# Kernel optimization log

Measured on AMD Instinct MI355X. Metric: run time of the kernel, lower is better.

## Reference

```python
import jax, jax.numpy as jnp
import numpy as np

EPS = 1e-8


def setup_inputs() -> dict:
    key = jax.random.key(0)
    k1, k2, k3, k4, k5 = jax.random.split(key, 5)
    N, B, T, D = 8, 2, 2048, 2048
    F = 4 * D
    blocks = jax.random.normal(k1, (N, B, T, D), dtype=jnp.float32)
    partial_block = jax.random.normal(k2, (B, T, D), dtype=jnp.float32)
    proj_w = jax.random.normal(k3, (D,), dtype=jnp.float32) * 0.02
    norm_scale = jnp.ones((D,), dtype=jnp.float32)
    ffn_w1 = jax.random.normal(k4, (D, F), dtype=jnp.float32) * 0.02
    ffn_w2 = jax.random.normal(k5, (F, D), dtype=jnp.float32) * 0.02
    return {
        "blocks": blocks,
        "partial_block": partial_block,
        "proj_w": proj_w,
        "norm_scale": norm_scale,
        "ffn_w1": ffn_w1,
        "ffn_w2": ffn_w2,
    }


def reference(blocks, partial_block, proj_w, norm_scale, ffn_w1, ffn_w2):
    # Stack completed blocks with current partial sum: V [N1, B, T, D]
    V = jnp.concatenate([blocks, partial_block[None]], axis=0)
    # RMSNorm over D (keys)
    rms = jnp.sqrt(jnp.mean(V * V, axis=-1, keepdims=True) + EPS)
    K = norm_scale * V / rms
    # Pseudo-query dot-product logits [N1, B, T], softmax over blocks (axis 0)
    logits = jnp.einsum('nbtd,d->nbt', K, proj_w)
    alpha = jax.nn.softmax(logits, axis=0)
    # Weighted sum of raw values -> new hidden state h [B, T, D]
    h = jnp.einsum('nbt,nbtd->btd', alpha, V)
    # Sublayer: standard FFN (D -> 4D gelu -> D)
    f_out = jax.nn.gelu(h @ ffn_w1) @ ffn_w2
    # layer_number % block_size != 0 branch: accumulate partial sum
    new_partial = partial_block + f_out
    return h, new_partial
```

## Files before the change

kernel.cpp:

```cpp
#include <hip/hip_runtime.h>

typedef unsigned short ushort_t;
typedef __bf16 bf16x8 __attribute__((ext_vector_type(8)));
typedef float f32x4 __attribute__((ext_vector_type(4)));

#define NB 8
#define BB 2
#define TT 2048
#define DD 2048
#define FF 8192
#define MM (BB * TT)
#define BTD ((size_t)BB * TT * DD)

__device__ __forceinline__ unsigned short f2bf(float f) {
  unsigned int u = __float_as_uint(f);
  u += 0x7FFFu + ((u >> 16) & 1u);
  return (unsigned short)(u >> 16);
}

__device__ __forceinline__ float gelu_tanh(float x) {
  float u = 0.7978845608028654f * (x + 0.044715f * x * x * x);
  float e = __expf(2.0f * u);
  float th = 1.0f - 2.0f / (e + 1.0f);
  return 0.5f * x * (1.0f + th);
}

#define ASYNC_COPY16(gp, lp)                                                   \
  __builtin_amdgcn_global_load_lds(                                            \
      (__attribute__((address_space(1))) void*)(gp),                           \
      (__attribute__((address_space(3))) void*)(lp), 16, 0, 0)

__global__ __launch_bounds__(256) void transpose_conv(
    const float* __restrict__ in, ushort_t* __restrict__ out, int R, int C) {
  __shared__ float tile[32][33];
  const int tx = threadIdx.x & 31, ty = threadIdx.x >> 5;
  const int r0 = blockIdx.y * 32, c0 = blockIdx.x * 32;
#pragma unroll
  for (int i = 0; i < 32; i += 8)
    tile[ty + i][tx] = in[(size_t)(r0 + ty + i) * C + (c0 + tx)];
  __syncthreads();
#pragma unroll
  for (int i = 0; i < 32; i += 8)
    out[(size_t)(c0 + ty + i) * R + (r0 + tx)] = f2bf(tile[tx][ty + i]);
}

__global__ __launch_bounds__(256) void attn_fuse(
    const float* __restrict__ blocks, const float* __restrict__ partial,
    const float* __restrict__ proj_w, const float* __restrict__ norm_scale,
    float* __restrict__ h_out, ushort_t* __restrict__ h_bf) {
  const int t = threadIdx.x;
  const int bt = blockIdx.x;
  const size_t rowoff = (size_t)bt * DD;
  const int d0 = t * 4;

  float w[8];
  {
    float4 ns = *(const float4*)(norm_scale + d0);
    float4 pw = *(const float4*)(proj_w + d0);
    w[0] = ns.x * pw.x; w[1] = ns.y * pw.y; w[2] = ns.z * pw.z; w[3] = ns.w * pw.w;
    ns = *(const float4*)(norm_scale + 1024 + d0);
    pw = *(const float4*)(proj_w + 1024 + d0);
    w[4] = ns.x * pw.x; w[5] = ns.y * pw.y; w[6] = ns.z * pw.z; w[7] = ns.w * pw.w;
  }

  float ss[9], dt[9];
#pragma unroll
  for (int n = 0; n < 9; ++n) {
    const float* rp = (n < 8) ? (blocks + (size_t)n * BTD + rowoff)
                              : (partial + rowoff);
    float4 v0 = *(const float4*)(rp + d0);
    float4 v1 = *(const float4*)(rp + 1024 + d0);
    ss[n] = v0.x * v0.x + v0.y * v0.y + v0.z * v0.z + v0.w * v0.w +
            v1.x * v1.x + v1.y * v1.y + v1.z * v1.z + v1.w * v1.w;
    dt[n] = v0.x * w[0] + v0.y * w[1] + v0.z * w[2] + v0.w * w[3] +
            v1.x * w[4] + v1.y * w[5] + v1.z * w[6] + v1.w * w[7];
  }

  __shared__ float red[2][9][4];
  const int lane = t & 63, wv = t >> 6;
#pragma unroll
  for (int n = 0; n < 9; ++n) {
    float a = ss[n], c = dt[n];
#pragma unroll
    for (int off = 32; off > 0; off >>= 1) {
      a += __shfl_down(a, off, 64);
      c += __shfl_down(c, off, 64);
    }
    if (lane == 0) { red[0][n][wv] = a; red[1][n][wv] = c; }
  }
  __syncthreads();
  __shared__ float logit_s[9];
  if (t < 9) {
    float a = red[0][t][0] + red[0][t][1] + red[0][t][2] + red[0][t][3];
    float c = red[1][t][0] + red[1][t][1] + red[1][t][2] + red[1][t][3];
    logit_s[t] = c * rsqrtf(a * (1.0f / (float)DD) + 1e-8f);
  }
  __syncthreads();

  float lg[9], mx = -1e30f;
#pragma unroll
  for (int n = 0; n < 9; ++n) { lg[n] = logit_s[n]; mx = fmaxf(mx, lg[n]); }
  float den = 0.0f;
#pragma unroll
  for (int n = 0; n < 9; ++n) { lg[n] = __expf(lg[n] - mx); den += lg[n]; }
  const float inv = 1.0f / den;

  float h[8] = {0, 0, 0, 0, 0, 0, 0, 0};
#pragma unroll
  for (int n = 0; n < 9; ++n) {
    const float* rp = (n < 8) ? (blocks + (size_t)n * BTD + rowoff)
                              : (partial + rowoff);
    float4 v0 = *(const float4*)(rp + d0);
    float4 v1 = *(const float4*)(rp + 1024 + d0);
    const float a = lg[n] * inv;
    h[0] += a * v0.x; h[1] += a * v0.y; h[2] += a * v0.z; h[3] += a * v0.w;
    h[4] += a * v1.x; h[5] += a * v1.y; h[6] += a * v1.z; h[7] += a * v1.w;
  }

  float4 o0 = {h[0], h[1], h[2], h[3]}, o1 = {h[4], h[5], h[6], h[7]};
  *(float4*)(h_out + rowoff + d0) = o0;
  *(float4*)(h_out + rowoff + 1024 + d0) = o1;
  uint2 p0, p1;
  p0.x = (unsigned)f2bf(h[0]) | ((unsigned)f2bf(h[1]) << 16);
  p0.y = (unsigned)f2bf(h[2]) | ((unsigned)f2bf(h[3]) << 16);
  p1.x = (unsigned)f2bf(h[4]) | ((unsigned)f2bf(h[5]) << 16);
  p1.y = (unsigned)f2bf(h[6]) | ((unsigned)f2bf(h[7]) << 16);
  *(uint2*)(h_bf + rowoff + d0) = p0;
  *(uint2*)(h_bf + rowoff + 1024 + d0) = p1;
}

template <int BN, int EPI>
__global__ __launch_bounds__(512) void gemm256(
    const ushort_t* __restrict__ A, const ushort_t* __restrict__ BT,
    const int K, const int N, const int GX, ushort_t* __restrict__ Cb,
    const float* __restrict__ addend, float* __restrict__ Cf) {
  constexpr int BM = 256;
  constexpr int WCN = BN / 4;
  constexpr int MF = 8;
  constexpr int NF = WCN / 16;
  constexpr int MH = 4;
  constexpr int CH_B = BN / 128;
  constexpr int ABYTES = BM * 64 * 2;

  __shared__ __align__(16) ushort_t lds0[(BM + BN) * 64];
  __shared__ __align__(16) ushort_t lds1[(BM + BN) * 64];

  const int t = threadIdx.x;
  const int lane = t & 63, wv = t >> 6;
  const int wr = wv >> 2, wc = wv & 3;
  const int fr = lane & 15;

  const int nwg = gridDim.x;
  const int wg = blockIdx.x;
  const int swz = (wg & 7) * (nwg >> 3) + (wg >> 3);
  const int bx = swz % GX, by = swz / GX;
  const int row0 = by * BM, col0 = bx * BN;

  const int sr = t >> 3;
  const int scolb = ((t & 7) * 16) ^ ((sr & 7) << 4);
  const ushort_t* gA = A + (size_t)(row0 + sr) * K + (scolb >> 1);
  const ushort_t* gB = BT + (size_t)(col0 + sr) * K + (scolb >> 1);

#define STAGE(DST, KT)                                                         \
  {                                                                            \
    const int _k0 = (KT)*64;                                                   \
    for (int j = 0; j < 4; ++j)                                                \
      ASYNC_COPY16(gA + (size_t)(j * 64) * K + _k0,                            \
                   &DST[j * 4096 + wv * 512]);                                 \
    for (int j = 0; j < 2 * CH_B; ++j)                                         \
      ASYNC_COPY16(gB + (size_t)(j * 64) * K + _k0,                            \
                   &DST[BM * 64 + j * 4096 + wv * 512]);                       \
  }

  const int s_lane = (fr & 7) << 4;
  const int offk0 = ((lane >> 4) * 16) ^ s_lane;
  const int offk1 = (64 + (lane >> 4) * 16) ^ s_lane;
  const int aoffA = (wr * 128 + fr) * 128;
  int boffB[NF];
#pragma unroll
  for (int n = 0; n < NF; ++n)
    boffB[n] = ABYTES + (wc * WCN + n * 16 + fr) * 128;

  f32x4 acc[MF][NF];
#pragma unroll
  for (int m = 0; m < MF; ++m)
#pragma unroll
    for (int n = 0; n < NF; ++n) {
      f32x4 z = {0.f, 0.f, 0.f, 0.f};
      acc[m][n] = z;
    }

#define TILE(SRC, DST, STAGEKT, DOSTAGE)                                       \
  {                                                                            \
    const char* _L = (const char*)SRC;                                         \
    bf16x8 bfr[NF], afr[MH];                                                   \
                                                     \
    for (int n = 0; n < NF; ++n)                                               \
      bfr[n] = *(const bf16x8*)(_L + boffB[n] + offk0);                        \
    for (int m = 0; m < MH; ++m)                                               \
      afr[m] = *(const bf16x8*)(_L + aoffA + m * 2048 + offk0);                \
    if (DOSTAGE) STAGE(DST, STAGEKT);                                          \
    __builtin_amdgcn_s_barrier();                                              \
    __builtin_amdgcn_s_setprio(1);                                             \
    for (int m = 0; m < MH; ++m)                                               \
      for (int n = 0; n < NF; ++n)                                             \
        acc[m][n] = __builtin_amdgcn_mfma_f32_16x16x32_bf16(afr[m], bfr[n],    \
                                                            acc[m][n], 0, 0, 0); \
    __builtin_amdgcn_s_setprio(0);                                             \
    __builtin_amdgcn_s_barrier();                                              \
                                                     \
    for (int m = 0; m < MH; ++m)                                               \
      afr[m] = *(const bf16x8*)(_L + aoffA + (MH + m) * 2048 + offk0);         \
    __builtin_amdgcn_s_barrier();                                              \
    __builtin_amdgcn_s_setprio(1);                                             \
    for (int m = 0; m < MH; ++m)                                               \
      for (int n = 0; n < NF; ++n)                                             \
        acc[MH + m][n] = __builtin_amdgcn_mfma_f32_16x16x32_bf16(              \
            afr[m], bfr[n], acc[MH + m][n], 0, 0, 0);                          \
    __builtin_amdgcn_s_setprio(0);                                             \
    __builtin_amdgcn_s_barrier();                                              \
                                                     \
    for (int n = 0; n < NF; ++n)                                               \
      bfr[n] = *(const bf16x8*)(_L + boffB[n] + offk1);                        \
    for (int m = 0; m < MH; ++m)                                               \
      afr[m] = *(const bf16x8*)(_L + aoffA + m * 2048 + offk1);                \
    __builtin_amdgcn_s_barrier();                                              \
    __builtin_amdgcn_s_setprio(1);                                             \
    for (int m = 0; m < MH; ++m)                                               \
      for (int n = 0; n < NF; ++n)                                             \
        acc[m][n] = __builtin_amdgcn_mfma_f32_16x16x32_bf16(afr[m], bfr[n],    \
                                                            acc[m][n], 0, 0, 0); \
    __builtin_amdgcn_s_setprio(0);                                             \
    __builtin_amdgcn_s_barrier();                                              \
                                                     \
    for (int m = 0; m < MH; ++m)                                               \
      afr[m] = *(const bf16x8*)(_L + aoffA + (MH + m) * 2048 + offk1);         \
    __builtin_amdgcn_s_barrier();                                              \
    __builtin_amdgcn_s_setprio(1);                                             \
    for (int m = 0; m < MH; ++m)                                               \
      for (int n = 0; n < NF; ++n)                                             \
        acc[MH + m][n] = __builtin_amdgcn_mfma_f32_16x16x32_bf16(              \
            afr[m], bfr[n], acc[MH + m][n], 0, 0, 0);                          \
    __builtin_amdgcn_s_setprio(0);                                             \
    __syncthreads();        \
  }

  STAGE(lds0, 0);
  __syncthreads();

  const int NT = K >> 6;
  for (int kt = 0; kt < NT; kt += 2) {
    TILE(lds0, lds1, kt + 1, (kt + 1 < NT));
    TILE(lds1, lds0, kt + 2, (kt + 2 < NT));
  }

  const int r4 = (lane >> 4) * 4;
#pragma unroll
  for (int m = 0; m < MF; ++m) {
    const int grow = row0 + wr * 128 + m * 16 + r4;
#pragma unroll
    for (int n = 0; n < NF; ++n) {
      const int gcol = col0 + wc * WCN + n * 16 + fr;
#pragma unroll
      for (int r = 0; r < 4; ++r) {
        const float v = acc[m][n][r];
        const size_t idx = (size_t)(grow + r) * N + gcol;
        if (EPI == 0) {
          Cb[idx] = f2bf(gelu_tanh(v));
        } else {
          Cf[idx] = v + addend[idx];
        }
      }
    }
  }
#undef TILE
#undef STAGE
}

extern "C" void kernel_launch(void* const* d_in, const int* in_sizes, int n_in,
                              void* d_out, int out_size, void* d_ws,
                              size_t ws_size, hipStream_t stream) {
  const float* blocks = (const float*)d_in[0];
  const float* partial = (const float*)d_in[1];
  const float* proj_w = (const float*)d_in[2];
  const float* norm_scale = (const float*)d_in[3];
  const float* w1 = (const float*)d_in[4];
  const float* w2 = (const float*)d_in[5];

  float* out = (float*)d_out;
  float* h_out = out;
  float* new_partial = out + BTD;

  char* ws = (char*)d_ws;
  ushort_t* h_bf = (ushort_t*)ws;
  ushort_t* w1T = (ushort_t*)(ws + (size_t)16777216);
  ushort_t* w2T = (ushort_t*)(ws + (size_t)16777216 + 33554432);
  ushort_t* act = (ushort_t*)(ws + (size_t)16777216 + 2 * 33554432ull);

  transpose_conv<<<dim3(FF / 32, DD / 32), 256, 0, stream>>>(w1, w1T, DD, FF);
  transpose_conv<<<dim3(DD / 32, FF / 32), 256, 0, stream>>>(w2, w2T, FF, DD);

  attn_fuse<<<MM, 256, 0, stream>>>(blocks, partial, proj_w, norm_scale, h_out,
                                    h_bf);

  gemm256<256, 0><<<(FF / 256) * (MM / 256), 512, 0, stream>>>(
      h_bf, w1T, DD, FF, FF / 256, act, nullptr, nullptr);
  gemm256<128, 1><<<(DD / 128) * (MM / 256), 512, 0, stream>>>(
      act, w2T, FF, DD, DD / 128, nullptr, partial, new_partial);
}
```

Measured before the change: 423.4 us.

## Split async tile loads into quadrant-ordered chunks with partial vmcnt waits

Measured after the change: 426.9 us. No clear change (+0.8%).

```diff
diff --git a/kernel.cpp b/kernel.cpp
--- a/kernel.cpp
+++ b/kernel.cpp
@@ -23,6 +23,14 @@
   float e = __expf(2.0f * u);
   float th = 1.0f - 2.0f / (e + 1.0f);
   return 0.5f * x * (1.0f + th);
+}
+
+template <int N>
+__device__ __forceinline__ void wait_vmcnt() {
+  if constexpr (N == 0) asm volatile("s_waitcnt vmcnt(0)" ::: "memory");
+  else if constexpr (N == 2) asm volatile("s_waitcnt vmcnt(2)" ::: "memory");
+  else if constexpr (N == 4) asm volatile("s_waitcnt vmcnt(4)" ::: "memory");
+  else if constexpr (N == 6) asm volatile("s_waitcnt vmcnt(6)" ::: "memory");
 }
 
 #define ASYNC_COPY16(gp, lp)                                                   \
@@ -138,9 +146,10 @@
   constexpr int WCN = BN / 4;
   constexpr int MF = 8;
   constexpr int NF = WCN / 16;
-  constexpr int MH = 4;
-  constexpr int CH_B = BN / 128;
-  constexpr int ABYTES = BM * 64 * 2;
+  constexpr int NH = NF / 2;
+  constexpr int NCB = BN / 64;
+  constexpr int AUS = BM * 64;
+  constexpr int WP2 = (BN == 256) ? 6 : 4;
 
   __shared__ __align__(16) ushort_t lds0[(BM + BN) * 64];
   __shared__ __align__(16) ushort_t lds1[(BM + BN) * 64];
@@ -161,16 +170,11 @@
   const ushort_t* gA = A + (size_t)(row0 + sr) * K + (scolb >> 1);
   const ushort_t* gB = BT + (size_t)(col0 + sr) * K + (scolb >> 1);
 
-#define STAGE(DST, KT)                                                         \
-  {                                                                            \
-    const int _k0 = (KT)*64;                                                   \
-    for (int j = 0; j < 4; ++j)                                                \
-      ASYNC_COPY16(gA + (size_t)(j * 64) * K + _k0,                            \
-                   &DST[j * 4096 + wv * 512]);                                 \
-    for (int j = 0; j < 2 * CH_B; ++j)                                         \
-      ASYNC_COPY16(gB + (size_t)(j * 64) * K + _k0,                            \
-                   &DST[BM * 64 + j * 4096 + wv * 512]);                       \
-  }
+#define STAGE_A(W, c, KT)                                                      \
+  ASYNC_COPY16(gA + (size_t)((c)*64) * K + (KT)*64, &W[(c)*4096 + wv * 512])
+#define STAGE_B(W, c, KT)                                                      \
+  ASYNC_COPY16(gB + (size_t)((c)*64) * K + (KT)*64,                            \
+               &W[AUS + (c)*4096 + wv * 512])
 
   const int s_lane = (fr & 7) << 4;
   const int offk0 = ((lane >> 4) * 16) ^ s_lane;
@@ -179,7 +183,7 @@
   int boffB[NF];
 #pragma unroll
   for (int n = 0; n < NF; ++n)
-    boffB[n] = ABYTES + (wc * WCN + n * 16 + fr) * 128;
+    boffB[n] = AUS * 2 + (wc * WCN + n * 16 + fr) * 128;
 
   f32x4 acc[MF][NF];
 #pragma unroll
@@ -190,68 +194,93 @@
       acc[m][n] = z;
     }
 
-#define TILE(SRC, DST, STAGEKT, DOSTAGE)                                       \
+#define MFMA_(a, b, c) __builtin_amdgcn_mfma_f32_16x16x32_bf16(a, b, c, 0, 0, 0)
+
+#define TILE(Rb, Wb, KT, S)                                                    \
   {                                                                            \
-    const char* _L = (const char*)SRC;                                         \
-    bf16x8 bfr[NF], afr[MH];                                                   \
-                                                     \
-    for (int n = 0; n < NF; ++n)                                               \
-      bfr[n] = *(const bf16x8*)(_L + boffB[n] + offk0);                        \
-    for (int m = 0; m < MH; ++m)                                               \
-      afr[m] = *(const bf16x8*)(_L + aoffA + m * 2048 + offk0);                \
-    if (DOSTAGE) STAGE(DST, STAGEKT);                                          \
+    const char* _L = (const char*)Rb;                                          \
+    bf16x8 af[4][2], b0[NH][2], b1[NH][2];                                     \
+                                                 \
+    _Pragma("unroll") for (int m = 0; m < 4; ++m) {                            \
+      af[m][0] = *(const bf16x8*)(_L + aoffA + m * 2048 + offk0);              \
+      af[m][1] = *(const bf16x8*)(_L + aoffA + m * 2048 + offk1);              \
+    }                                                                          \
+    _Pragma("unroll") for (int n = 0; n < NH; ++n) {                           \
+      b0[n][0] = *(const bf16x8*)(_L + boffB[n] + offk0);                      \
+      b0[n][1] = *(const bf16x8*)(_L + boffB[n] + offk1);                      \
+    }                                                                          \
+    if (S) {                                                                   \
+      STAGE_A(Wb, 0, KT); STAGE_A(Wb, 2, KT);                                  \
+      STAGE_B(Wb, 0, KT); STAGE_B(Wb, 1, KT);                                  \
+    }                                                                          \
     __builtin_amdgcn_s_barrier();                                              \
     __builtin_amdgcn_s_setprio(1);                                             \
-    for (int m = 0; m < MH; ++m)                                               \
-      for (int n = 0; n < NF; ++n)                                             \
-        acc[m][n] = __builtin_amdgcn_mfma_f32_16x16x32_bf16(afr[m], bfr[n],    \
-                                                            acc[m][n], 0, 0, 0); \
+    _Pragma("unroll") for (int m = 0; m < 4; ++m)                              \
+      _Pragma("unroll") for (int n = 0; n < NH; ++n) {                         \
+        acc[m][n] = MFMA_(af[m][0], b0[n][0], acc[m][n]);                      \
+        acc[m][n] = MFMA_(af[m][1], b0[n][1], acc[m][n]);                      \
+      }                                                                        \
     __builtin_amdgcn_s_setprio(0);                                             \
     __builtin_amdgcn_s_barrier();                                              \
-                                                     \
-    for (int m = 0; m < MH; ++m)                                               \
-      afr[m] = *(const bf16x8*)(_L + aoffA + (MH + m) * 2048 + offk0);         \
+                                                 \
+    _Pragma("unroll") for (int n = 0; n < NH; ++n) {                           \
+      b1[n][0] = *(const bf16x8*)(_L + boffB[NH + n] + offk0);                 \
+      b1[n][1] = *(const bf16x8*)(_L + boffB[NH + n] + offk1);                 \
+    }                                                                          \
+    if (S && BN == 256) { STAGE_B(Wb, 2, KT); STAGE_B(Wb, 3, KT); }            \
     __builtin_amdgcn_s_barrier();                                              \
     __builtin_amdgcn_s_setprio(1);                                             \
-    for (int m = 0; m < MH; ++m)                                               \
-      for (int n = 0; n < NF; ++n)                                             \
-        acc[MH + m][n] = __builtin_amdgcn_mfma_f32_16x16x32_bf16(              \
-            afr[m], bfr[n], acc[MH + m][n], 0, 0, 0);                          \
+    _Pragma("unroll") for (int m = 0; m < 4; ++m)                              \
+      _Pragma("unroll") for (int n = 0; n < NH; ++n) {                         \
+        acc[m][NH + n] = MFMA_(af[m][0], b1[n][0], acc[m][NH + n]);            \
+        acc[m][NH + n] = MFMA_(af[m][1], b1[n][1], acc[m][NH + n]);            \
+      }                                                                        \
     __builtin_amdgcn_s_setprio(0);                                             \
-    __builtin_amdgcn_s_barrier();                                              \
-                                                     \
-    for (int n = 0; n < NF; ++n)                                               \
-      bfr[n] = *(const bf16x8*)(_L + boffB[n] + offk1);                        \
-    for (int m = 0; m < MH; ++m)                                               \
-      afr[m] = *(const bf16x8*)(_L + aoffA + m * 2048 + offk1);                \
+    if (S) wait_vmcnt<WP2>(); else wait_vmcnt<0>();                            \
+    __builtin_amdgcn_s_barrier();                                              \
+                                                 \
+    _Pragma("unroll") for (int m = 0; m < 4; ++m) {                            \
+      af[m][0] = *(const bf16x8*)(_L + aoffA + (4 + m) * 2048 + offk0);        \
+      af[m][1] = *(const bf16x8*)(_L + aoffA + (4 + m) * 2048 + offk1);        \
+    }                                                                          \
+    if (S) { STAGE_A(Wb, 1, KT); STAGE_A(Wb, 3, KT); }                         \
     __builtin_amdgcn_s_barrier();                                              \
     __builtin_amdgcn_s_setprio(1);                                             \
-    for (int m = 0; m < MH; ++m)                                               \
-      for (int n = 0; n < NF; ++n)                                             \
-        acc[m][n] = __builtin_amdgcn_mfma_f32_16x16x32_bf16(afr[m], bfr[n],    \
-                                                            acc[m][n], 0, 0, 0); \
+    _Pragma("unroll") for (int m = 0; m < 4; ++m)                              \
+      _Pragma("unroll") for (int n = 0; n < NH; ++n) {                         \
+        acc[4 + m][NH + n] = MFMA_(af[m][0], b1[n][0], acc[4 + m][NH + n]);    \
+        acc[4 + m][NH + n] = MFMA_(af[m][1], b1[n][1], acc[4 + m][NH + n]);    \
+      }                                                                        \
     __builtin_amdgcn_s_setprio(0);                                             \
     __builtin_amdgcn_s_barrier();                                              \
-                                                     \
-    for (int m = 0; m < MH; ++m)                                               \
-      afr[m] = *(const bf16x8*)(_L + aoffA + (MH + m) * 2048 + offk1);         \
+                                  \
+    _Pragma("unroll") for (int n = 0; n < NH; ++n) {                           \
+      b0[n][0] = *(const bf16x8*)(_L + boffB[n] + offk0);                      \
+      b0[n][1] = *(const bf16x8*)(_L + boffB[n] + offk1);                      \
+    }                                                                          \
     __builtin_amdgcn_s_barrier();                                              \
     __builtin_amdgcn_s_setprio(1);                                             \
-    for (int m = 0; m < MH; ++m)                                               \
-      for (int n = 0; n < NF; ++n)                                             \
-        acc[MH + m][n] = __builtin_amdgcn_mfma_f32_16x16x32_bf16(              \
-            afr[m], bfr[n], acc[MH + m][n], 0, 0, 0);                          \
+    _Pragma("unroll") for (int m = 0; m < 4; ++m)                              \
+      _Pragma("unroll") for (int n = 0; n < NH; ++n) {                         \
+        acc[4 + m][n] = MFMA_(af[m][0], b0[n][0], acc[4 + m][n]);              \
+        acc[4 + m][n] = MFMA_(af[m][1], b0[n][1], acc[4 + m][n]);              \
+      }                                                                        \
     __builtin_amdgcn_s_setprio(0);                                             \
-    __syncthreads();        \
-  }
-
-  STAGE(lds0, 0);
-  __syncthreads();
+    if (S) wait_vmcnt<2>();                                                    \
+    __builtin_amdgcn_s_barrier();                                              \
+  }
+
+  STAGE_A(lds0, 0, 0); STAGE_A(lds0, 2, 0);
+  STAGE_B(lds0, 0, 0); STAGE_B(lds0, 1, 0);
+  if (BN == 256) { STAGE_B(lds0, 2, 0); STAGE_B(lds0, 3, 0); }
+  STAGE_A(lds0, 1, 0); STAGE_A(lds0, 3, 0);
+  wait_vmcnt<2>();
+  __builtin_amdgcn_s_barrier();
 
   const int NT = K >> 6;
   for (int kt = 0; kt < NT; kt += 2) {
-    TILE(lds0, lds1, kt + 1, (kt + 1 < NT));
-    TILE(lds1, lds0, kt + 2, (kt + 2 < NT));
+    TILE(lds0, lds1, kt + 1, (kt + 1) < NT);
+    TILE(lds1, lds0, kt + 2, (kt + 2) < NT);
   }
 
   const int r4 = (lane >> 4) * 4;
@@ -274,7 +303,9 @@
     }
   }
 #undef TILE
-#undef STAGE
+#undef MFMA_
+#undef STAGE_A
+#undef STAGE_B
 }
 
 extern "C" void kernel_launch(void* const* d_in, const int* in_sizes, int n_in,
```
